# Performance work log

Measured on AMD Instinct MI355X. Metric: run time of the kernel, lower is better.

The kernel has to match this reference:

```python
import jax, jax.numpy as jnp
import numpy as np

B, S, D = 4, 2048, 1024
H, DH = 16, 64
THETA = 10000.0


def _rope_tables(seq_len, dim):
    # freqs_cis = exp(i * t * f), here as cos/sin tables, shape [S, dim//2]
    freqs = 1.0 / (THETA ** (jnp.arange(0, dim, 2, dtype=jnp.float32) / dim))
    ang = jnp.outer(jnp.arange(seq_len, dtype=jnp.float32), freqs)
    return jnp.cos(ang), jnp.sin(ang)


def _apply_rope(x, cos, sin):
    # x: [B,S,H,DH]; pairs are interleaved (x[...,2i], x[...,2i+1])
    xe = x[..., 0::2]
    xo = x[..., 1::2]
    c = cos[None, :, None, :]
    s = sin[None, :, None, :]
    out = jnp.stack([xe * c - xo * s, xe * s + xo * c], axis=-1)
    return out.reshape(x.shape).astype(x.dtype)


def setup_inputs() -> dict:
    key = jax.random.key(0)
    ks = jax.random.split(key, 5)
    x = jax.random.normal(ks[0], (B, S, D), dtype=jnp.float32)
    Wq = jax.random.normal(ks[1], (D, D), dtype=jnp.float32) * 0.02
    Wk = jax.random.normal(ks[2], (D, D), dtype=jnp.float32) * 0.02
    Wv = jax.random.normal(ks[3], (D, D), dtype=jnp.float32) * 0.02
    Wo = jax.random.normal(ks[4], (D, D), dtype=jnp.float32) * 0.02
    lambdas = jnp.zeros((2,), dtype=jnp.float32)
    return {"x": x, "Wq": Wq, "Wk": Wk, "Wv": Wv, "Wo": Wo, "lambdas": lambdas}


def reference(x, Wq, Wk, Wv, Wo, lambdas):
    scale = 1.0 / np.sqrt(DH)
    q = (x @ Wq.T).reshape(B, S, H, DH)
    k = (x @ Wk.T).reshape(B, S, H, DH)
    v = (x @ Wv.T).reshape(B, S, H, DH)
    cos, sin = _rope_tables(S, DH)
    q = _apply_rope(q, cos, sin)
    k = _apply_rope(k, cos, sin)
    # explicit QK^T with causal mask, softmax, then @V (dropout is identity in eval)
    attn = jnp.einsum('bshd,bthd->bhst', q, k) * scale  # [B,H,S,S]
    causal = jnp.tril(jnp.ones((S, S), dtype=bool))
    attn = jnp.where(causal[None, None], attn, -jnp.inf)
    probs = jax.nn.softmax(attn, axis=-1)
    head_out = jnp.einsum('bhst,bthd->bshd', probs, v)  # [B,S,H,DH]
    out = head_out.reshape(B, S, D) @ Wo.T
    return out
```

## Files before the change

### kernel.cpp

```cpp
#include <hip/hip_runtime.h>
#include <math.h>

static constexpr int Bsz = 4, Sq = 2048, Dm = 1024, NH = 16, DHd = 64;
static constexpr int Mrows = Bsz * Sq;
static constexpr float ROPE_LN = 0.14391156831212787f;

typedef _Float16 half8 __attribute__((ext_vector_type(8)));
typedef _Float16 half4v __attribute__((ext_vector_type(4)));
typedef float f32x4 __attribute__((ext_vector_type(4)));

__device__ __forceinline__ void gl_lds16(const void* g, void* l) {
    __builtin_amdgcn_global_load_lds(
        (const __attribute__((address_space(1))) void*)g,
        (__attribute__((address_space(3))) void*)l, 16, 0, 0);
}

__global__ __launch_bounds__(256) void prep_kernel(
    const float* __restrict__ x,
    const float* __restrict__ Wq, const float* __restrict__ Wk,
    const float* __restrict__ Wv, const float* __restrict__ Wo,
    _Float16* __restrict__ xh,
    _Float16* __restrict__ Wqh, _Float16* __restrict__ Wkh,
    _Float16* __restrict__ Wvh, _Float16* __restrict__ Woh,
    float2* __restrict__ rope)
{
    const int i = blockIdx.x * 256 + threadIdx.x;
    if (i < 2097152) {
        const float4 v = ((const float4*)x)[i];
        half4v hv;
        hv[0] = (_Float16)v.x; hv[1] = (_Float16)v.y;
        hv[2] = (_Float16)v.z; hv[3] = (_Float16)v.w;
        ((half4v*)xh)[i] = hv;
    } else if (i < 3145728) {
        const int w = (i - 2097152) >> 18;
        const int off = (i - 2097152) & 262143;
        const float* s = (w == 0) ? Wq : (w == 1) ? Wk : (w == 2) ? Wv : Wo;
        _Float16* d = (w == 0) ? Wqh : (w == 1) ? Wkh : (w == 2) ? Wvh : Woh;
        const float sc = (w == 0) ? 0.125f : 1.0f;
        const float4 v = ((const float4*)s)[off];
        half4v hv;
        hv[0] = (_Float16)(v.x * sc); hv[1] = (_Float16)(v.y * sc);
        hv[2] = (_Float16)(v.z * sc); hv[3] = (_Float16)(v.w * sc);
        ((half4v*)d)[off] = hv;
    } else {
        const int t = i - 3145728;
        const int pos = t >> 5, j = t & 31;
        const float f = expf(-ROPE_LN * (float)(2 * j));
        const float a = (float)pos * f;
        rope[t] = make_float2(cosf(a), sinf(a));
    }
}

template <typename OutT, int MODE>
__device__ __forceinline__ void mfma_gemm_body(
    const _Float16* __restrict__ A, const _Float16* __restrict__ W,
    OutT* __restrict__ C, const float2* __restrict__ rope, int K, int N)
{
    __shared__ _Float16 As[128 * 32];
    __shared__ _Float16 Bs[128 * 32];

    const int tid = threadIdx.x;
    const int wave = tid >> 6, lane = tid & 63;
    const int quad = lane >> 4, l16 = lane & 15;
    const int wm = (wave >> 1) * 64, wn = (wave & 1) * 64;
    const int m0 = blockIdx.y * 128, n0 = blockIdx.x * 128;

    const _Float16* gA[2]; const _Float16* gB[2];
    _Float16* lA[2]; _Float16* lB[2];
    #pragma unroll
    for (int i = 0; i < 2; ++i) {
        const int F = (wave * 2 + i) * 64 + lane;
        const int r = F >> 2, cp = F & 3;
        const int c = cp ^ ((r >> 1) & 3);
        gA[i] = A + (size_t)(m0 + r) * K + c * 8;
        gB[i] = W + (size_t)(n0 + r) * K + c * 8;
        lA[i] = As + (wave * 2 + i) * 512;
        lB[i] = Bs + (wave * 2 + i) * 512;
    }

    const int sw = (l16 >> 1) & 3;
    int offA[4], offB[4];
    #pragma unroll
    for (int t = 0; t < 4; ++t) {
        offA[t] = (wm + t * 16 + l16) * 32 + ((quad ^ sw) * 8);
        offB[t] = (wn + t * 16 + l16) * 32 + ((quad ^ sw) * 8);
    }

    f32x4 acc[4][4];
    #pragma unroll
    for (int im = 0; im < 4; ++im)
        #pragma unroll
        for (int nb = 0; nb < 4; ++nb)
            #pragma unroll
            for (int r = 0; r < 4; ++r) acc[im][nb][r] = 0.f;

    for (int k0 = 0; k0 < K; k0 += 32) {
        __syncthreads();
        #pragma unroll
        for (int i = 0; i < 2; ++i) {
            gl_lds16(gA[i] + k0, lA[i]);
            gl_lds16(gB[i] + k0, lB[i]);
        }
        __syncthreads();

        half8 a[4], b[4];
        #pragma unroll
        for (int t = 0; t < 4; ++t) {
            a[t] = *(const half8*)&As[offA[t]];
            b[t] = *(const half8*)&Bs[offB[t]];
        }
        #pragma unroll
        for (int im = 0; im < 4; ++im)
            #pragma unroll
            for (int nb = 0; nb < 4; ++nb)
                acc[im][nb] = __builtin_amdgcn_mfma_f32_16x16x32_f16(
                    a[im], b[nb], acc[im][nb], 0, 0, 0);
    }

    #pragma unroll
    for (int nb = 0; nb < 4; ++nb) {
        const int n = n0 + wn + nb * 16 + l16;
        const int j = (n & 63) >> 1;
        #pragma unroll
        for (int im = 0; im < 4; ++im) {
            #pragma unroll
            for (int r = 0; r < 4; ++r) {
                const int m = m0 + wm + im * 16 + quad * 4 + r;
                float v = acc[im][nb][r];
                if constexpr (MODE == 1) {
                    const int pos = m & (Sq - 1);
                    const float2 cs = rope[pos * 32 + j];
                    const float vp = __shfl_xor(v, 1);
                    v = (n & 1) ? (vp * cs.y + v * cs.x)
                                : (v * cs.x - vp * cs.y);
                    C[(size_t)m * N + n] = (_Float16)v;
                } else if constexpr (MODE == 2) {
                    const int hb = (m >> 11) * 16 + (n >> 6);
                    const int dh = n & 63;
                    const int t = m & (Sq - 1);
                    const int tt = t & 63;
                    const int c = ((tt & 15) << 2) + (tt >> 4);
                    C[(((size_t)hb * 64 + dh) << 11) + (t & ~63) + c] =
                        (_Float16)v;
                } else {
                    C[(size_t)m * N + n] = v;
                }
            }
        }
    }
}

__global__ __launch_bounds__(256) void qkv_mfma_kernel(
    const _Float16* __restrict__ xh,
    const _Float16* __restrict__ Wq, const _Float16* __restrict__ Wk,
    const _Float16* __restrict__ Wv,
    _Float16* __restrict__ Qo, _Float16* __restrict__ Ko,
    _Float16* __restrict__ VTp, const float2* __restrict__ rope)
{
    const int z = blockIdx.z;
    if (z == 0)
        mfma_gemm_body<_Float16, 1>(xh, Wq, Qo, rope, Dm, Dm);
    else if (z == 1)
        mfma_gemm_body<_Float16, 1>(xh, Wk, Ko, rope, Dm, Dm);
    else
        mfma_gemm_body<_Float16, 2>(xh, Wv, VTp, nullptr, Dm, Dm);
}

__global__ __launch_bounds__(256) void oproj_mfma_kernel(
    const _Float16* __restrict__ HOh, const _Float16* __restrict__ Wo,
    float* __restrict__ out)
{
    mfma_gemm_body<float, 0>(HOh, Wo, out, nullptr, Dm, Dm);
}

__global__ __launch_bounds__(256) void attn_mfma_kernel(
    const _Float16* __restrict__ Q, const _Float16* __restrict__ K,
    const _Float16* __restrict__ VT, _Float16* __restrict__ HO)
{
    __shared__ _Float16 Ks[64 * 64];
    __shared__ _Float16 Vs[64 * 64];
    __shared__ _Float16 Ps[4][16][72];

    const int tid = threadIdx.x;
    const int wave = tid >> 6, lane = tid & 63;
    const int quad = lane >> 4, l16 = lane & 15;
    const int id = blockIdx.x;
    const int hb = id & 63;
    const int qi = 31 - (id >> 6);
    const int h = hb & 15, b = hb >> 4;
    const int q0 = qi * 64;
    const size_t base = (size_t)b * Sq * Dm + (size_t)h * DHd;
    const size_t vtbase = (size_t)hb * 64 * Sq;

    half8 ones;
    #pragma unroll
    for (int i = 0; i < 8; ++i) ones[i] = (_Float16)1.0f;

    half8 aQ[2];
    {
        const _Float16* qrow =
            Q + base + (size_t)(q0 + wave * 16 + l16) * Dm + quad * 8;
        aQ[0] = *(const half8*)(qrow);
        aQ[1] = *(const half8*)(qrow + 32);
    }

    f32x4 Oacc[4];
    #pragma unroll
    for (int nb = 0; nb < 4; ++nb)
        #pragma unroll
        for (int r = 0; r < 4; ++r) Oacc[nb][r] = 0.f;
    f32x4 lacc;
    #pragma unroll
    for (int r = 0; r < 4; ++r) lacc[r] = 0.f;

    auto do_tile = [&](int t0, bool diag) {
        __syncthreads();

        #pragma unroll
        for (int i = 0; i < 2; ++i) {
            const int F = (wave * 2 + i) * 64 + lane;
            const int r = F >> 3;
            const int cl = (F & 7) ^ (r & 7);
            gl_lds16(K + base + (size_t)(t0 + r) * Dm + cl * 8,
                     Ks + (wave * 2 + i) * 512);
            gl_lds16(VT + vtbase + ((size_t)r << 11) + t0 + cl * 8,
                     Vs + (wave * 2 + i) * 512);
        }
        __syncthreads();

        f32x4 sacc[4];
        #pragma unroll
        for (int nb = 0; nb < 4; ++nb)
            #pragma unroll
            for (int r = 0; r < 4; ++r) sacc[nb][r] = 0.f;
        #pragma unroll
        for (int kstep = 0; kstep < 2; ++kstep) {
            #pragma unroll
            for (int nb = 0; nb < 4; ++nb) {
                const int krow = nb * 16 + l16;
                const int kch = (kstep * 4 + quad) ^ (krow & 7);
                const half8 bK = *(const half8*)&Ks[krow * 64 + kch * 8];
                sacc[nb] = __builtin_amdgcn_mfma_f32_16x16x32_f16(
                    aQ[kstep], bK, sacc[nb], 0, 0, 0);
            }
        }

        #pragma unroll
        for (int r = 0; r < 4; ++r) {
            half4v pk;
            #pragma unroll
            for (int nb = 0; nb < 4; ++nb) {
                float v = sacc[nb][r];
                if (diag && (nb * 16 + l16 > wave * 16 + quad * 4 + r))
                    v = -1.0e4f;
                pk[nb] = (_Float16)__expf(v);
            }
            *(half4v*)&Ps[wave][quad * 4 + r][l16 * 4] = pk;
        }

        #pragma unroll
        for (int kstep = 0; kstep < 2; ++kstep) {
            const half8 aP =
                *(const half8*)&Ps[wave][l16][kstep * 32 + quad * 8];
            lacc = __builtin_amdgcn_mfma_f32_16x16x32_f16(
                aP, ones, lacc, 0, 0, 0);
            #pragma unroll
            for (int nb = 0; nb < 4; ++nb) {
                const int vrow = nb * 16 + l16;
                const int vch = (kstep * 4 + quad) ^ (vrow & 7);
                const half8 bV = *(const half8*)&Vs[vrow * 64 + vch * 8];
                Oacc[nb] = __builtin_amdgcn_mfma_f32_16x16x32_f16(
                    aP, bV, Oacc[nb], 0, 0, 0);
            }
        }
    };

    for (int jt = 0; jt < qi; ++jt) do_tile(jt * 64, false);
    do_tile(q0, true);

    float inv[4];
    #pragma unroll
    for (int r = 0; r < 4; ++r) inv[r] = 1.0f / lacc[r];
    #pragma unroll
    for (int nb = 0; nb < 4; ++nb)
        #pragma unroll
        for (int r = 0; r < 4; ++r) {
            const int row = wave * 16 + quad * 4 + r;
            HO[base + (size_t)(q0 + row) * Dm + nb * 16 + l16] =
                (_Float16)(Oacc[nb][r] * inv[r]);
        }
}

extern "C" void kernel_launch(void* const* d_in, const int* in_sizes, int n_in,
                              void* d_out, int out_size, void* d_ws, size_t ws_size,
                              hipStream_t stream)
{
    const float* x  = (const float*)d_in[0];
    const float* Wq = (const float*)d_in[1];
    const float* Wk = (const float*)d_in[2];
    const float* Wv = (const float*)d_in[3];
    const float* Wo = (const float*)d_in[4];
    float* out = (float*)d_out;

    const size_t matX = (size_t)Mrows * Dm;
    const size_t matW = (size_t)Dm * Dm;

    _Float16* xh  = (_Float16*)d_ws;
    _Float16* Wqh = xh + matX;
    _Float16* Wkh = Wqh + matW;
    _Float16* Wvh = Wkh + matW;
    _Float16* Woh = Wvh + matW;
    _Float16* Qh  = Woh + matW;
    _Float16* Kh  = Qh + matX;
    _Float16* VTp = Kh + matX;
    _Float16* HOh = VTp + matX;
    float2* rope  = (float2*)(HOh + matX);

    dim3 blk(256);
    prep_kernel<<<(3145728 + 65536) / 256, blk, 0, stream>>>(
        x, Wq, Wk, Wv, Wo, xh, Wqh, Wkh, Wvh, Woh, rope);
    qkv_mfma_kernel<<<dim3(Dm / 128, Mrows / 128, 3), blk, 0, stream>>>(
        xh, Wqh, Wkh, Wvh, Qh, Kh, VTp, rope);
    attn_mfma_kernel<<<dim3(32 * NH * Bsz), blk, 0, stream>>>(
        Qh, Kh, VTp, HOh);
    oproj_mfma_kernel<<<dim3(Dm / 128, Mrows / 128, 1), blk, 0, stream>>>(
        HOh, Woh, out);
}
```

Before: 265.2 us.

## Double-buffer LDS tiles in GEMM and attention, vectorize transposed V stores

Both the projection GEMM and the attention kernel now keep two LDS buffers. The next K-slice, or the next K/V tile, is issued through global_load_lds before computing on the current buffer, so global-to-LDS traffic overlaps with MFMA work and there is one barrier per stage instead of two. The V-projection epilogue also packs 16 fp16 results per lane into two 16-byte stores, matching the existing permuted VT layout, instead of scattered 2-byte stores. The cost is twice the LDS per block, which may lower occupancy.

Result: slower. 271.2 us (+2.3%).

```diff
diff --git a/kernel.cpp b/kernel.cpp
--- a/kernel.cpp
+++ b/kernel.cpp
@@ -56,8 +56,8 @@
     const _Float16* __restrict__ A, const _Float16* __restrict__ W,
     OutT* __restrict__ C, const float2* __restrict__ rope, int K, int N)
 {
-    __shared__ _Float16 As[128 * 32];
-    __shared__ _Float16 Bs[128 * 32];
+    __shared__ _Float16 As[2][128 * 32];
+    __shared__ _Float16 Bs[2][128 * 32];
 
     const int tid = threadIdx.x;
     const int wave = tid >> 6, lane = tid & 63;
@@ -66,7 +66,7 @@
     const int m0 = blockIdx.y * 128, n0 = blockIdx.x * 128;
 
     const _Float16* gA[2]; const _Float16* gB[2];
-    _Float16* lA[2]; _Float16* lB[2];
+    int lOff[2];
     #pragma unroll
     for (int i = 0; i < 2; ++i) {
         const int F = (wave * 2 + i) * 64 + lane;
@@ -74,8 +74,7 @@
         const int c = cp ^ ((r >> 1) & 3);
         gA[i] = A + (size_t)(m0 + r) * K + c * 8;
         gB[i] = W + (size_t)(n0 + r) * K + c * 8;
-        lA[i] = As + (wave * 2 + i) * 512;
-        lB[i] = Bs + (wave * 2 + i) * 512;
+        lOff[i] = (wave * 2 + i) * 512;
     }
 
     const int sw = (l16 >> 1) & 3;
@@ -94,20 +93,19 @@
             #pragma unroll
             for (int r = 0; r < 4; ++r) acc[im][nb][r] = 0.f;
 
-    for (int k0 = 0; k0 < K; k0 += 32) {
-        __syncthreads();
+    auto stage = [&](int buf, int koff) {
         #pragma unroll
         for (int i = 0; i < 2; ++i) {
-            gl_lds16(gA[i] + k0, lA[i]);
-            gl_lds16(gB[i] + k0, lB[i]);
-        }
-        __syncthreads();
-
+            gl_lds16(gA[i] + koff, &As[buf][lOff[i]]);
+            gl_lds16(gB[i] + koff, &Bs[buf][lOff[i]]);
+        }
+    };
+    auto compute = [&](int buf) {
         half8 a[4], b[4];
         #pragma unroll
         for (int t = 0; t < 4; ++t) {
-            a[t] = *(const half8*)&As[offA[t]];
-            b[t] = *(const half8*)&Bs[offB[t]];
+            a[t] = *(const half8*)&As[buf][offA[t]];
+            b[t] = *(const half8*)&Bs[buf][offB[t]];
         }
         #pragma unroll
         for (int im = 0; im < 4; ++im)
@@ -115,35 +113,56 @@
             for (int nb = 0; nb < 4; ++nb)
                 acc[im][nb] = __builtin_amdgcn_mfma_f32_16x16x32_f16(
                     a[im], b[nb], acc[im][nb], 0, 0, 0);
+    };
+
+    stage(0, 0);
+
+    for (int k0 = 0; k0 < K; k0 += 64) {
+        __syncthreads();
+        stage(1, k0 + 32);
+        compute(0);
+        __syncthreads();
+        if (k0 + 64 < K) stage(0, k0 + 64);
+        compute(1);
     }
 
     #pragma unroll
     for (int nb = 0; nb < 4; ++nb) {
         const int n = n0 + wn + nb * 16 + l16;
-        const int j = (n & 63) >> 1;
-        #pragma unroll
-        for (int im = 0; im < 4; ++im) {
-            #pragma unroll
-            for (int r = 0; r < 4; ++r) {
-                const int m = m0 + wm + im * 16 + quad * 4 + r;
-                float v = acc[im][nb][r];
-                if constexpr (MODE == 1) {
-                    const int pos = m & (Sq - 1);
-                    const float2 cs = rope[pos * 32 + j];
-                    const float vp = __shfl_xor(v, 1);
-                    v = (n & 1) ? (vp * cs.y + v * cs.x)
-                                : (v * cs.x - vp * cs.y);
-                    C[(size_t)m * N + n] = (_Float16)v;
-                } else if constexpr (MODE == 2) {
-                    const int hb = (m >> 11) * 16 + (n >> 6);
-                    const int dh = n & 63;
-                    const int t = m & (Sq - 1);
-                    const int tt = t & 63;
-                    const int c = ((tt & 15) << 2) + (tt >> 4);
-                    C[(((size_t)hb * 64 + dh) << 11) + (t & ~63) + c] =
-                        (_Float16)v;
-                } else {
-                    C[(size_t)m * N + n] = v;
+        if constexpr (MODE == 2) {
+            const int hb = ((m0 + wm) >> 11) * 16 + (n >> 6);
+            const int dh = n & 63;
+            const int tb = (m0 + wm) & (Sq - 1);
+            half8 v0, v1;
+            #pragma unroll
+            for (int r = 0; r < 4; ++r)
+                #pragma unroll
+                for (int im = 0; im < 4; ++im) {
+                    const int idx = r * 4 + im;
+                    const _Float16 h = (_Float16)acc[im][nb][r];
+                    if (idx < 8) v0[idx] = h; else v1[idx - 8] = h;
+                }
+            _Float16* dst = C + (((size_t)hb * 64 + dh) << 11) + tb + quad * 16;
+            *(half8*)dst = v0;
+            *(half8*)(dst + 8) = v1;
+        } else {
+            const int j = (n & 63) >> 1;
+            #pragma unroll
+            for (int im = 0; im < 4; ++im) {
+                #pragma unroll
+                for (int r = 0; r < 4; ++r) {
+                    const int m = m0 + wm + im * 16 + quad * 4 + r;
+                    float v = acc[im][nb][r];
+                    if constexpr (MODE == 1) {
+                        const int pos = m & (Sq - 1);
+                        const float2 cs = rope[pos * 32 + j];
+                        const float vp = __shfl_xor(v, 1);
+                        v = (n & 1) ? (vp * cs.y + v * cs.x)
+                                    : (v * cs.x - vp * cs.y);
+                        C[(size_t)m * N + n] = (_Float16)v;
+                    } else {
+                        C[(size_t)m * N + n] = v;
+                    }
                 }
             }
         }
@@ -177,8 +196,8 @@
     const _Float16* __restrict__ Q, const _Float16* __restrict__ K,
     const _Float16* __restrict__ VT, _Float16* __restrict__ HO)
 {
-    __shared__ _Float16 Ks[64 * 64];
-    __shared__ _Float16 Vs[64 * 64];
+    __shared__ _Float16 Ks[2][64 * 64];
+    __shared__ _Float16 Vs[2][64 * 64];
     __shared__ _Float16 Ps[4][16][72];
 
     const int tid = threadIdx.x;
@@ -213,20 +232,22 @@
     #pragma unroll
     for (int r = 0; r < 4; ++r) lacc[r] = 0.f;
 
-    auto do_tile = [&](int t0, bool diag) {
-        __syncthreads();
-
+    auto stage_tile = [&](int t0, int buf) {
         #pragma unroll
         for (int i = 0; i < 2; ++i) {
             const int F = (wave * 2 + i) * 64 + lane;
             const int r = F >> 3;
             const int cl = (F & 7) ^ (r & 7);
             gl_lds16(K + base + (size_t)(t0 + r) * Dm + cl * 8,
-                     Ks + (wave * 2 + i) * 512);
+                     &Ks[buf][(wave * 2 + i) * 512]);
             gl_lds16(VT + vtbase + ((size_t)r << 11) + t0 + cl * 8,
-                     Vs + (wave * 2 + i) * 512);
-        }
-        __syncthreads();
+                     &Vs[buf][(wave * 2 + i) * 512]);
+        }
+    };
+
+    auto do_tile = [&](int buf, bool diag) {
+        const _Float16* Kb = Ks[buf];
+        const _Float16* Vb = Vs[buf];
 
         f32x4 sacc[4];
         #pragma unroll
@@ -239,7 +260,7 @@
             for (int nb = 0; nb < 4; ++nb) {
                 const int krow = nb * 16 + l16;
                 const int kch = (kstep * 4 + quad) ^ (krow & 7);
-                const half8 bK = *(const half8*)&Ks[krow * 64 + kch * 8];
+                const half8 bK = *(const half8*)&Kb[krow * 64 + kch * 8];
                 sacc[nb] = __builtin_amdgcn_mfma_f32_16x16x32_f16(
                     aQ[kstep], bK, sacc[nb], 0, 0, 0);
             }
@@ -268,15 +289,19 @@
             for (int nb = 0; nb < 4; ++nb) {
                 const int vrow = nb * 16 + l16;
                 const int vch = (kstep * 4 + quad) ^ (vrow & 7);
-                const half8 bV = *(const half8*)&Vs[vrow * 64 + vch * 8];
+                const half8 bV = *(const half8*)&Vb[vrow * 64 + vch * 8];
                 Oacc[nb] = __builtin_amdgcn_mfma_f32_16x16x32_f16(
                     aP, bV, Oacc[nb], 0, 0, 0);
             }
         }
     };
 
-    for (int jt = 0; jt < qi; ++jt) do_tile(jt * 64, false);
-    do_tile(q0, true);
+    stage_tile(0, 0);
+    for (int t = 0; t <= qi; ++t) {
+        __syncthreads();
+        if (t < qi) stage_tile((t + 1) * 64, (t + 1) & 1);
+        do_tile(t & 1, t == qi);
+    }
 
     float inv[4];
     #pragma unroll
```
